# Optimization experiments

Hardware: AMD Instinct MI355X
Metric: run time of the kernel (lower is better)

## Reference

```python
import jax, jax.numpy as jnp
import numpy as np

D = 32   # manifold_dim
H = 128  # hidden_dim
B = 32   # batch


def setup_inputs() -> dict:
    key = jax.random.key(0)
    ks = jax.random.split(key, 13)
    def lin(k, fan_in, shape):
        # torch nn.Linear default init: U(-1/sqrt(fan_in), 1/sqrt(fan_in))
        return jax.random.uniform(k, shape, jnp.float32, -1.0, 1.0) / np.float32(np.sqrt(fan_in))
    return {
        "points": jax.random.normal(ks[0], (B, D), jnp.float32),
        # metric_network: Linear(D,H) -> ReLU -> Linear(H, D*D)
        "mw1": lin(ks[1], D, (D, H)), "mb1": lin(ks[2], D, (H,)),
        "mw2": lin(ks[3], H, (H, D * D)), "mb2": lin(ks[4], H, (D * D,)),
        # christoffel_network: Linear(D+3,H) -> Tanh -> Linear(H,1)  (scalar output per (i,j,k))
        "cw1": lin(ks[5], D + 3, (D + 3, H)), "cb1": lin(ks[6], D + 3, (H,)),
        "cw2": lin(ks[7], H, (H,)), "cb2": lin(ks[8], H, ()),
        # ricci_network: Linear(2D+1, 2H) -> ReLU -> Linear(2H, 1)
        "rw1": lin(ks[9], 2 * D + 1, (2 * D + 1, 2 * H)), "rb1": lin(ks[10], 2 * D + 1, (2 * H,)),
        "rw2": lin(ks[11], 2 * H, (2 * H,)), "rb2": lin(ks[12], 2 * H, ()),
    }


def _forward(points, mw1, mb1, mw2, mb2, cw1, cb1, cw2, cb2, rw1, rb1, rw2, rb2):
    b, d = points.shape
    # metric tensor g: [b, d, d]
    metric = (jax.nn.relu(points @ mw1 + mb1) @ mw2 + mb2).reshape(b, d, d)

    # Christoffel MLP input per (i,j,k): cat([points, g_ij, g_jk, g_ki]) -> [b,d,d,d,d+3]
    gij = jnp.broadcast_to(metric[:, :, :, None], (b, d, d, d))                       # g[i,j]
    gjk = jnp.broadcast_to(metric[:, None, :, :], (b, d, d, d))                       # g[j,k]
    gki = jnp.broadcast_to(jnp.swapaxes(metric, 1, 2)[:, :, None, :], (b, d, d, d))   # g[k,i]
    pts = jnp.broadcast_to(points[:, None, None, None, :], (b, d, d, d, d))
    cin = jnp.concatenate([pts, gij[..., None], gjk[..., None], gki[..., None]], axis=-1)
    ch = jnp.tanh(jnp.einsum('bijkf,fh->bijkh', cin, cw1) + cb1)
    christoffel = jnp.einsum('bijkh,h->bijk', ch, cw2) + cb2                          # [b,d,d,d]

    # Ricci MLP input per (i,j): cat([points, g_ij, Gamma_ij[:]]) -> [b,d,d,2d+1]
    pts2 = jnp.broadcast_to(points[:, None, None, :], (b, d, d, d))
    rin = jnp.concatenate([pts2, metric[..., None], christoffel], axis=-1)
    rh = jax.nn.relu(jnp.einsum('bijf,fh->bijh', rin, rw1) + rb1)
    ricci = jnp.einsum('bijh,h->bij', rh, rw2) + rb2                                  # [b,d,d]
    return ricci


def reference(points, mw1, mb1, mw2, mb2, cw1, cb1, cw2, cb2, rw1, rb1, rw2, rb2):
    return _forward(points, mw1, mb1, mw2, mb2, cw1, cb1, cw2, cb2, rw1, rb1, rw2, rb2)
```

## Files before the change

### kernel.cpp

```cpp
#include <hip/hip_runtime.h>

#define D 32
#define H 128
#define TN 256
#define TRANGE 6.0f

typedef float v2f __attribute__((ext_vector_type(2)));

__global__ __launch_bounds__(256) void setup_kernel(
    const float* __restrict__ points,
    const float* __restrict__ mw1, const float* __restrict__ mb1,
    const float* __restrict__ mw2, const float* __restrict__ mb2,
    const float* __restrict__ cw1, const float* __restrict__ cb1,
    const float* __restrict__ rw1, const float* __restrict__ rb1,
    float* __restrict__ metric, float4* __restrict__ cpk4,
    float* __restrict__ rbase)
{
    __shared__ float p[D];
    __shared__ float h1[H];
    const int blk = blockIdx.x;
    const int b   = blk >> 3;
    const int q   = blk & 7;
    const int t   = threadIdx.x;
    if (t < D) p[t] = points[b * D + t];
    __syncthreads();

    if (t < H) {
        float acc = mb1[t];
        #pragma unroll
        for (int d = 0; d < D; ++d) acc = fmaf(p[d], mw1[d * H + t], acc);
        h1[t] = fmaxf(acc, 0.0f);
    }

    if (q == 0 && t < H) {
        constexpr float S = (float)TN / (2.0f * TRANGE);
        float cacc = cb1[t];
        #pragma unroll
        for (int d = 0; d < D; ++d) cacc = fmaf(p[d], cw1[d * H + t], cacc);
        cpk4[b * H + t] = make_float4(S * cacc + (float)(TN / 2),
                                      S * cw1[32 * H + t],
                                      S * cw1[33 * H + t],
                                      S * cw1[34 * H + t]);
    }
    if (q == 1) {
        float racc = rb1[t];
        #pragma unroll
        for (int d = 0; d < D; ++d) racc = fmaf(p[d], rw1[d * 256 + t], racc);
        rbase[b * 256 + t] = racc;
    }
    __syncthreads();

    if (t < 128) {
        const int m = q * 128 + t;
        float acc = mb2[m];
        #pragma unroll 8
        for (int h = 0; h < H; ++h) acc = fmaf(h1[h], mw2[h * 1024 + m], acc);
        metric[b * 1024 + m] = acc;
    }
}

__global__ __launch_bounds__(128) void christoffel_kernel(
    const float* __restrict__ metric,
    const float4* __restrict__ cpk4, const float* __restrict__ cw2,
    const float* __restrict__ cb2,
    float* __restrict__ gamma)
{
    __shared__ float2 tab[TN];
    const int blk = blockIdx.x;
    const int b   = blk >> 7;
    const int i   = (blk >> 2) & 31;
    const int q   = blk & 3;
    const int t   = threadIdx.x;

    constexpr float hstep = 2.0f * TRANGE / (float)TN;
    constexpr float Kc = 2.8853900817779268f;
    #pragma unroll
    for (int e = 0; e < TN / 128; ++e) {
        const int idx = e * 128 + t;
        const float x0 = -TRANGE + idx * hstep;
        const float e0 = __builtin_amdgcn_exp2f(Kc * x0);
        const float v0 = 1.0f - 2.0f * __builtin_amdgcn_rcpf(e0 + 1.0f);
        const float e1 = __builtin_amdgcn_exp2f(Kc * (x0 + hstep));
        const float v1 = 1.0f - 2.0f * __builtin_amdgcn_rcpf(e1 + 1.0f);
        tab[idx] = make_float2(v0, v1 - v0);
    }

    const int r0 = q * 256 + t * 2;
    const int j  = r0 >> 5;
    const int k0 = r0 & 31;
    const float* __restrict__ Mb = metric + b * 1024;
    const float gij  = Mb[i * 32 + j];
    const float gjk0 = Mb[j * 32 + k0];
    const float gjk1 = Mb[j * 32 + k0 + 1];
    const float gki0 = Mb[k0 * 32 + i];
    const float gki1 = Mb[(k0 + 1) * 32 + i];
    __syncthreads();

    float acc0 = 0.0f, acc1 = 0.0f;
    const float4* __restrict__ cp = cpk4 + b * H;

    #pragma unroll 8
    for (int h = 0; h < H; ++h) {
        const float4 c = cp[h];
        const float w = cw2[h];
        const float pre = fmaf(gij, c.y, c.x);
        float u0 = fmaf(gki0, c.w, fmaf(gjk0, c.z, pre));
        float u1 = fmaf(gki1, c.w, fmaf(gjk1, c.z, pre));
        u0 = __builtin_amdgcn_fmed3f(u0, 0.0f, 255.0f);
        u1 = __builtin_amdgcn_fmed3f(u1, 0.0f, 255.0f);
        const int i0 = (int)u0;
        const int i1 = (int)u1;
        const float fr0 = u0 - (float)i0;
        const float fr1 = u1 - (float)i1;
        const float2 p0 = tab[i0];
        const float2 p1 = tab[i1];
        acc0 = fmaf(fmaf(fr0, p0.y, p0.x), w, acc0);
        acc1 = fmaf(fmaf(fr1, p1.y, p1.x), w, acc1);
    }

    const float bias = cb2[0];
    v2f res; res.x = acc0 + bias; res.y = acc1 + bias;
    *((v2f*)(gamma + ((b * 32 + i) * 32 + j) * 32 + k0)) = res;
}

__global__ __launch_bounds__(256) void ricci_kernel(
    const float* __restrict__ metric, const float* __restrict__ rbase,
    const float* __restrict__ rw1, const float* __restrict__ rw2,
    const float* __restrict__ rb2,
    const float* __restrict__ gamma,
    float* __restrict__ out)
{
    __shared__ float red[4][16];
    const int blk = blockIdx.x;
    const int bi  = blk >> 1;
    const int b   = blk >> 6;
    const int i   = (blk >> 1) & 31;
    const int jh  = blk & 1;
    const int t   = threadIdx.x;

    float w[33];
    #pragma unroll
    for (int f = 0; f < 33; ++f) w[f] = rw1[(32 + f) * 256 + t];
    const float rbv   = rbase[b * 256 + t];
    const float wo    = rw2[t];
    const float rbias = rb2[0];

    const float4* __restrict__ G4   = (const float4*)(gamma + bi * 1024 + jh * 512);
    const float*  __restrict__ Mrow = metric + b * 1024 + i * 32 + jh * 16;

    const int wid  = t >> 6;
    const int lane = t & 63;

    #pragma unroll 2
    for (int jp = 0; jp < 8; ++jp) {
        float pp[2];
        #pragma unroll
        for (int s = 0; s < 2; ++s) {
            const int jj = jp * 2 + s;
            v2f hA = (v2f)(0.0f), hB = (v2f)(0.0f);
            #pragma unroll
            for (int k4 = 0; k4 < 8; ++k4) {
                const float4 g = G4[jj * 8 + k4];
                v2f glo; glo.x = g.x; glo.y = g.y;
                v2f ghi; ghi.x = g.z; ghi.y = g.w;
                v2f wlo; wlo.x = w[k4 * 4 + 1]; wlo.y = w[k4 * 4 + 2];
                v2f whi; whi.x = w[k4 * 4 + 3]; whi.y = w[k4 * 4 + 4];
                hA = glo * wlo + hA;
                hB = ghi * whi + hB;
            }
            const float hid = fmaf(Mrow[jj], w[0], rbv) + (hA.x + hA.y) + (hB.x + hB.y);
            pp[s] = fmaxf(hid, 0.0f) * wo;
        }
        const float t0 = pp[0] + __shfl_xor(pp[0], 1);
        const float t1 = pp[1] + __shfl_xor(pp[1], 1);
        float z = (lane & 1) ? t1 : t0;
        #pragma unroll
        for (int off = 2; off < 64; off <<= 1) z += __shfl_xor(z, off);
        if (lane < 2) red[wid][jp * 2 + lane] = z;
    }
    __syncthreads();
    if (t < 16) out[bi * 32 + jh * 16 + t] = red[0][t] + red[1][t] + red[2][t] + red[3][t] + rbias;
}

extern "C" void kernel_launch(void* const* d_in, const int* in_sizes, int n_in,
                              void* d_out, int out_size, void* d_ws, size_t ws_size,
                              hipStream_t stream) {
    const float* points = (const float*)d_in[0];
    const float* mw1 = (const float*)d_in[1];
    const float* mb1 = (const float*)d_in[2];
    const float* mw2 = (const float*)d_in[3];
    const float* mb2 = (const float*)d_in[4];
    const float* cw1 = (const float*)d_in[5];
    const float* cb1 = (const float*)d_in[6];
    const float* cw2 = (const float*)d_in[7];
    const float* cb2 = (const float*)d_in[8];
    const float* rw1 = (const float*)d_in[9];
    const float* rb1 = (const float*)d_in[10];
    const float* rw2 = (const float*)d_in[11];
    const float* rb2 = (const float*)d_in[12];
    float* out = (float*)d_out;

    char* ws = (char*)d_ws;
    float*  metric = (float*)(ws);
    float4* cpk4   = (float4*)(ws + 131072);
    float*  rbase  = (float*)(ws + 196608);
    float*  gamma  = (float*)(ws + 262144);

    setup_kernel<<<256, 256, 0, stream>>>(points, mw1, mb1, mw2, mb2,
                                          cw1, cb1, rw1, rb1,
                                          metric, cpk4, rbase);
    christoffel_kernel<<<4096, 128, 0, stream>>>(metric, cpk4, cw2, cb2, gamma);
    ricci_kernel<<<2048, 256, 0, stream>>>(metric, rbase, rw1, rw2, rb2, gamma, out);
}
```

Measured before the change: 57.50 us.

## Process four k per thread in christoffel and pack cw2 into coefficient records

The christoffel kernel now computes four outputs per thread with 256-thread blocks, one block per (b,i), instead of two outputs per thread across four blocks. This amortises the per-h coefficient load and the tanh-table construction over more work. cw2 is folded into a 32-byte coefficient record so each h needs one vector load. The ricci inner loop now uses 32-byte loads and a single serial FMA chain instead of two paired accumulators. In exchange there are fewer blocks, higher register pressure, and a longer dependency chain in ricci.

```diff
diff --git a/kernel.cpp b/kernel.cpp
--- a/kernel.cpp
+++ b/kernel.cpp
@@ -6,14 +6,16 @@
 #define TRANGE 6.0f
 
 typedef float v2f __attribute__((ext_vector_type(2)));
+typedef float v8f __attribute__((ext_vector_type(8)));
 
 __global__ __launch_bounds__(256) void setup_kernel(
     const float* __restrict__ points,
     const float* __restrict__ mw1, const float* __restrict__ mb1,
     const float* __restrict__ mw2, const float* __restrict__ mb2,
     const float* __restrict__ cw1, const float* __restrict__ cb1,
+    const float* __restrict__ cw2,
     const float* __restrict__ rw1, const float* __restrict__ rb1,
-    float* __restrict__ metric, float4* __restrict__ cpk4,
+    float* __restrict__ metric, v8f* __restrict__ cpk8,
     float* __restrict__ rbase)
 {
     __shared__ float p[D];
@@ -37,10 +39,14 @@
         float cacc = cb1[t];
         #pragma unroll
         for (int d = 0; d < D; ++d) cacc = fmaf(p[d], cw1[d * H + t], cacc);
-        cpk4[b * H + t] = make_float4(S * cacc + (float)(TN / 2),
-                                      S * cw1[32 * H + t],
-                                      S * cw1[33 * H + t],
-                                      S * cw1[34 * H + t]);
+        v8f c;
+        c[0] = S * cacc + (float)(TN / 2);
+        c[1] = S * cw1[32 * H + t];
+        c[2] = S * cw1[33 * H + t];
+        c[3] = S * cw1[34 * H + t];
+        c[4] = cw2[t];
+        c[5] = 0.0f; c[6] = 0.0f; c[7] = 0.0f;
+        cpk8[b * H + t] = c;
     }
     if (q == 1) {
         float racc = rb1[t];
@@ -59,68 +65,62 @@
     }
 }
 
-__global__ __launch_bounds__(128) void christoffel_kernel(
+__global__ __launch_bounds__(256) void christoffel_kernel(
     const float* __restrict__ metric,
-    const float4* __restrict__ cpk4, const float* __restrict__ cw2,
-    const float* __restrict__ cb2,
+    const v8f* __restrict__ cpk8, const float* __restrict__ cb2,
     float* __restrict__ gamma)
 {
     __shared__ float2 tab[TN];
     const int blk = blockIdx.x;
-    const int b   = blk >> 7;
-    const int i   = (blk >> 2) & 31;
-    const int q   = blk & 3;
+    const int b   = blk >> 5;
+    const int i   = blk & 31;
     const int t   = threadIdx.x;
 
     constexpr float hstep = 2.0f * TRANGE / (float)TN;
     constexpr float Kc = 2.8853900817779268f;
-    #pragma unroll
-    for (int e = 0; e < TN / 128; ++e) {
-        const int idx = e * 128 + t;
-        const float x0 = -TRANGE + idx * hstep;
+    if (t < TN) {
+        const float x0 = -TRANGE + t * hstep;
         const float e0 = __builtin_amdgcn_exp2f(Kc * x0);
         const float v0 = 1.0f - 2.0f * __builtin_amdgcn_rcpf(e0 + 1.0f);
         const float e1 = __builtin_amdgcn_exp2f(Kc * (x0 + hstep));
         const float v1 = 1.0f - 2.0f * __builtin_amdgcn_rcpf(e1 + 1.0f);
-        tab[idx] = make_float2(v0, v1 - v0);
-    }
-
-    const int r0 = q * 256 + t * 2;
+        tab[t] = make_float2(v0, v1 - v0);
+    }
+
+    const int r0 = t * 4;
     const int j  = r0 >> 5;
     const int k0 = r0 & 31;
     const float* __restrict__ Mb = metric + b * 1024;
-    const float gij  = Mb[i * 32 + j];
-    const float gjk0 = Mb[j * 32 + k0];
-    const float gjk1 = Mb[j * 32 + k0 + 1];
-    const float gki0 = Mb[k0 * 32 + i];
-    const float gki1 = Mb[(k0 + 1) * 32 + i];
-    __syncthreads();
-
-    float acc0 = 0.0f, acc1 = 0.0f;
-    const float4* __restrict__ cp = cpk4 + b * H;
-
-    #pragma unroll 8
+    const float gij = Mb[i * 32 + j];
+    float gjk[4], gki[4], acc[4];
+    #pragma unroll
+    for (int r = 0; r < 4; ++r) {
+        gjk[r] = Mb[j * 32 + k0 + r];
+        gki[r] = Mb[(k0 + r) * 32 + i];
+        acc[r] = 0.0f;
+    }
+    __syncthreads();
+
+    const v8f* __restrict__ cp = cpk8 + b * H;
+
+    #pragma unroll 4
     for (int h = 0; h < H; ++h) {
-        const float4 c = cp[h];
-        const float w = cw2[h];
-        const float pre = fmaf(gij, c.y, c.x);
-        float u0 = fmaf(gki0, c.w, fmaf(gjk0, c.z, pre));
-        float u1 = fmaf(gki1, c.w, fmaf(gjk1, c.z, pre));
-        u0 = __builtin_amdgcn_fmed3f(u0, 0.0f, 255.0f);
-        u1 = __builtin_amdgcn_fmed3f(u1, 0.0f, 255.0f);
-        const int i0 = (int)u0;
-        const int i1 = (int)u1;
-        const float fr0 = u0 - (float)i0;
-        const float fr1 = u1 - (float)i1;
-        const float2 p0 = tab[i0];
-        const float2 p1 = tab[i1];
-        acc0 = fmaf(fmaf(fr0, p0.y, p0.x), w, acc0);
-        acc1 = fmaf(fmaf(fr1, p1.y, p1.x), w, acc1);
+        const v8f c = cp[h];
+        const float pre = fmaf(gij, c[1], c[0]);
+        #pragma unroll
+        for (int r = 0; r < 4; ++r) {
+            float u = fmaf(gki[r], c[3], fmaf(gjk[r], c[2], pre));
+            u = __builtin_amdgcn_fmed3f(u, 0.0f, (float)(TN - 1));
+            const int   iu = (int)u;
+            const float fr = u - (float)iu;
+            const float2 pv = tab[iu];
+            acc[r] = fmaf(fmaf(fr, pv.y, pv.x), c[4], acc[r]);
+        }
     }
 
     const float bias = cb2[0];
-    v2f res; res.x = acc0 + bias; res.y = acc1 + bias;
-    *((v2f*)(gamma + ((b * 32 + i) * 32 + j) * 32 + k0)) = res;
+    float4 res = make_float4(acc[0] + bias, acc[1] + bias, acc[2] + bias, acc[3] + bias);
+    *((float4*)(gamma + ((b * 32 + i) * 32 + j) * 32 + k0)) = res;
 }
 
 __global__ __launch_bounds__(256) void ricci_kernel(
@@ -145,8 +145,8 @@
     const float wo    = rw2[t];
     const float rbias = rb2[0];
 
-    const float4* __restrict__ G4   = (const float4*)(gamma + bi * 1024 + jh * 512);
-    const float*  __restrict__ Mrow = metric + b * 1024 + i * 32 + jh * 16;
+    const v8f*   __restrict__ G8   = (const v8f*)(gamma + bi * 1024 + jh * 512);
+    const float* __restrict__ Mrow = metric + b * 1024 + i * 32 + jh * 16;
 
     const int wid  = t >> 6;
     const int lane = t & 63;
@@ -157,18 +157,14 @@
         #pragma unroll
         for (int s = 0; s < 2; ++s) {
             const int jj = jp * 2 + s;
-            v2f hA = (v2f)(0.0f), hB = (v2f)(0.0f);
+            float hid = fmaf(Mrow[jj], w[0], rbv);
             #pragma unroll
-            for (int k4 = 0; k4 < 8; ++k4) {
-                const float4 g = G4[jj * 8 + k4];
-                v2f glo; glo.x = g.x; glo.y = g.y;
-                v2f ghi; ghi.x = g.z; ghi.y = g.w;
-                v2f wlo; wlo.x = w[k4 * 4 + 1]; wlo.y = w[k4 * 4 + 2];
-                v2f whi; whi.x = w[k4 * 4 + 3]; whi.y = w[k4 * 4 + 4];
-                hA = glo * wlo + hA;
-                hB = ghi * whi + hB;
+            for (int k8 = 0; k8 < 4; ++k8) {
+                const v8f g = G8[jj * 4 + k8];
+                #pragma unroll
+                for (int e = 0; e < 8; ++e)
+                    hid = fmaf(g[e], w[k8 * 8 + e + 1], hid);
             }
-            const float hid = fmaf(Mrow[jj], w[0], rbv) + (hA.x + hA.y) + (hB.x + hB.y);
             pp[s] = fmaxf(hid, 0.0f) * wo;
         }
         const float t0 = pp[0] + __shfl_xor(pp[0], 1);
@@ -201,14 +197,14 @@
     float* out = (float*)d_out;
 
     char* ws = (char*)d_ws;
-    float*  metric = (float*)(ws);
-    float4* cpk4   = (float4*)(ws + 131072);
-    float*  rbase  = (float*)(ws + 196608);
-    float*  gamma  = (float*)(ws + 262144);
+    float* metric = (float*)(ws);
+    v8f*   cpk8   = (v8f*)(ws + 131072);
+    float* rbase  = (float*)(ws + 262144);
+    float* gamma  = (float*)(ws + 294912);
 
     setup_kernel<<<256, 256, 0, stream>>>(points, mw1, mb1, mw2, mb2,
-                                          cw1, cb1, rw1, rb1,
-                                          metric, cpk4, rbase);
-    christoffel_kernel<<<4096, 128, 0, stream>>>(metric, cpk4, cw2, cb2, gamma);
+                                          cw1, cb1, cw2, rw1, rb1,
+                                          metric, cpk8, rbase);
+    christoffel_kernel<<<1024, 256, 0, stream>>>(metric, cpk8, cb2, gamma);
     ricci_kernel<<<2048, 256, 0, stream>>>(metric, rbase, rw1, rw2, rb2, gamma, out);
 }
```

Result: slower. 60.98 us (+6.1%).
